# Kernel optimization log

Measured on AMD Instinct MI355X. Metric: run time of the kernel, lower is better.

The kernel has to match this reference:

```python
import jax, jax.numpy as jnp
import numpy as np
from jax import lax

# SRCNN: conv 9x9 (1->64) + ReLU, conv 5x5 (64->32) + ReLU, conv 5x5 (32->1), same padding.
# 13 units total: indices 0-3 (x2 stage), 4-7 (x4 stage), 8-11 (x8 stage), 12 (msf).

def _conv(x, w, b):
    y = lax.conv_general_dilated(x, w, window_strides=(1, 1), padding='SAME',
                                 dimension_numbers=('NCHW', 'OIHW', 'NCHW'))
    return y + b[None, :, None, None]


def _srcnn(x, w1, b1, w2, b2, w3, b3):
    h = jax.nn.relu(_conv(x, w1, b1))
    h = jax.nn.relu(_conv(h, w2, b2))
    return _conv(h, w3, b3)


def _interleave(p0, p1, p2, p3):
    # out[b,c,2h,2w]=p0, out[b,c,2h,2w+1]=p1, out[b,c,2h+1,2w]=p2, out[b,c,2h+1,2w+1]=p3
    B, C, H, W = p0.shape
    x = jnp.stack([jnp.stack([p0, p1], axis=-1),
                   jnp.stack([p2, p3], axis=-1)], axis=-2)  # (B,C,H,W,2,2) dims (b,c,h,w,r,s)
    x = x.transpose(0, 1, 2, 4, 3, 5)                        # (b,c,h,r,w,s)
    return x.reshape(B, C, 2 * H, 2 * W)


def _stage(x, off, W1, B1, W2, B2, W3, B3):
    outs = [_srcnn(x, W1[off + i], B1[off + i], W2[off + i], B2[off + i],
                   W3[off + i], B3[off + i]) for i in range(4)]
    return _interleave(*outs)


def _upscale(x, s):
    B, C, H, W = x.shape
    return jax.image.resize(x, (B, C, H * s, W * s), method='bilinear')


def setup_inputs() -> dict:
    key = jax.random.key(0)
    ks = jax.random.split(key, 7)
    image = jax.random.normal(ks[0], (4, 1, 64, 64), dtype=jnp.float32)
    n = 13
    W1 = jax.random.normal(ks[1], (n, 64, 1, 9, 9), dtype=jnp.float32) * 0.05
    B1 = jnp.zeros((n, 64), dtype=jnp.float32)
    W2 = jax.random.normal(ks[2], (n, 32, 64, 5, 5), dtype=jnp.float32) * 0.05
    B2 = jnp.zeros((n, 32), dtype=jnp.float32)
    W3 = jax.random.normal(ks[3], (n, 1, 32, 5, 5), dtype=jnp.float32) * 0.05
    B3 = jnp.zeros((n, 1), dtype=jnp.float32)
    return {'image': image, 'W1': W1, 'B1': B1, 'W2': W2, 'B2': B2, 'W3': W3, 'B3': B3}


def reference(image, W1, B1, W2, B2, W3, B3):
    out_x2 = _stage(image, 0, W1, B1, W2, B2, W3, B3)   # (B,1,128,128)
    out_x4 = _stage(out_x2, 4, W1, B1, W2, B2, W3, B3)  # (B,1,256,256)
    out_x8 = _stage(out_x4, 8, W1, B1, W2, B2, W3, B3)  # (B,1,512,512)
    msf_in = _upscale(out_x2, 4) + _upscale(out_x4, 2) + out_x8
    msf_out = _srcnn(msf_in, W1[12], B1[12], W2[12], B2[12], W3[12], B3[12])
    return (out_x2, out_x4, out_x8, msf_out)
```

## Files before the change

### kernel.cpp

```cpp
#include <hip/hip_runtime.h>


typedef unsigned short ushort_t;
typedef __attribute__((ext_vector_type(8))) short short8;
typedef __attribute__((ext_vector_type(4))) float f32x4;
typedef __attribute__((ext_vector_type(2))) unsigned int u32x2;

__device__ __forceinline__ float us2f(ushort_t u) { return __uint_as_float(((unsigned int)u) << 16); }
__device__ __forceinline__ ushort_t f2us(float f) {
    unsigned int x = __float_as_uint(f);
    return (ushort_t)((x + 0x7fffu + ((x >> 16) & 1u)) >> 16);
}
__device__ __forceinline__ unsigned int pk_bf16(float lo, float hi) {
    unsigned int r;
    asm("v_cvt_pk_bf16_f32 %0, %1, %2" : "=v"(r) : "v"(lo), "v"(hi));
    return r;
}

#define MFMA16(a, b, c) __builtin_amdgcn_mfma_f32_16x16x32_bf16((a), (b), (c), 0, 0, 0)

__global__ __launch_bounds__(256) void prep_weights(
    const float* __restrict__ W1, const float* __restrict__ W2, const float* __restrict__ W3,
    ushort_t* __restrict__ w1t, ushort_t* __restrict__ w2t, ushort_t* __restrict__ w3t)
{
    int i = blockIdx.x * 256 + threadIdx.x;
    if (i < 13 * 3 * 4 * 64 * 8) {
        int e = i & 7, ch = (i >> 3) & 63, cig = (i >> 9) & 3;
        int r = i >> 11;
        int kc = r % 3, u = r / 3;
        int tap = kc * 32 + e * 4 + cig;
        w1t[i] = (tap < 81) ? f2us(W1[(u * 64 + ch) * 81 + tap]) : (ushort_t)0;
    }
    if (i < 665600) {
        int e = i & 7, co = (i >> 3) & 31, cig = (i >> 8) & 3;
        int r = i >> 10;
        int s = r % 25, cc = r / 25;
        int dx = s / 5, dy = s - 5 * dx;
        int c = cc & 1, u = cc >> 1;
        int tap = dy * 5 + dx;
        int ci = c * 32 + cig * 8 + e;
        w2t[i] = f2us(W2[((u * 32 + co) * 64 + ci) * 25 + tap]);
    }
    if (i < 13 * 25 * 32) {
        int ci = i & 31, r = i >> 5;
        int tap = r % 25, u = r / 25;
        w3t[i] = f2us(W3[(u * 32 + ci) * 25 + tap]);
    }
}

__global__ __launch_bounds__(256, 2) void srcnn_mfma(
    const float* __restrict__ in, int H, int W,
    const ushort_t* __restrict__ w1t, const ushort_t* __restrict__ w2t,
    const ushort_t* __restrict__ w3t,
    const float* __restrict__ gB1, const float* __restrict__ gB2,
    const float* __restrict__ gB3,
    int unitBase, float* __restrict__ out, int s2)
{
    __shared__ __align__(16) char smem[52928];
    ushort_t* sH1  = (ushort_t*)smem;
    ushort_t* sInU = (ushort_t*)(smem + 51328);
    ushort_t* sW3  = (ushort_t*)(smem + 51328);
    ushort_t* sH2  = (ushort_t*)smem;

    const int t = threadIdx.x, lane = t & 63, wv = t >> 6;
    const int q = lane >> 4, l15 = lane & 15;
    const int z = blockIdx.z;
    const int k4 = (s2 == 2) ? (z >> 2) : 0;
    const int b  = (s2 == 2) ? (z & 3)  : z;
    const int unit = unitBase + k4;
    const int ppx = k4 & 1, ppy = k4 >> 1;
    const int ox0 = blockIdx.x * 12, oy0 = blockIdx.y * 12;
    const int outW = W * s2;
    const int outH = H * s2;
    const float* inb = in + (size_t)b * H * W;

    const char* w2u = (const char*)w2t + (size_t)unit * 102400;

    auto loadB5 = [&](short8* buf, int p, int n) {
        const char* g = w2u + (size_t)p * 10240 + q * 512 + (n * 16 + l15) * 16;
#pragma unroll
        for (int dy = 0; dy < 5; ++dy)
            buf[dy] = *(const short8*)(g + dy * 2048);
    };

    for (int idx = t; idx < 784; idx += 256) {
        int y = idx / 28, x = idx - 28 * y;
        int gy = oy0 - 8 + y, gx = ox0 - 8 + x;
        sInU[idx] = (gy >= 0 && gy < H && gx >= 0 && gx < W)
                    ? f2us(inb[(size_t)gy * W + gx]) : (ushort_t)0;
    }
    __syncthreads();

    const ushort_t* w1u = w1t + (size_t)unit * (3 * 4 * 64 * 8);

    f32x4 bias4[4];
#pragma unroll
    for (int n = 0; n < 4; ++n)
        bias4[n] = *(const f32x4*)&gB1[unit * 64 + n * 16 + q * 4];

#pragma unroll 1
    for (int ms = 0; ms < 2; ++ms) {
        const int mbase = ms * 16;
        const int nim = ms ? 3 : 4;
        f32x4 acc1h[4][4];
#pragma unroll
        for (int i = 0; i < 4; ++i)
#pragma unroll
            for (int n = 0; n < 4; ++n) acc1h[i][n] = (f32x4){0.f, 0.f, 0.f, 0.f};

#pragma unroll 1
        for (int kc = 0; kc < 3; ++kc) {
            short8 bh[4];
#pragma unroll
            for (int n = 0; n < 4; ++n)
                bh[n] = *(const short8*)&w1u[((kc * 4 + q) * 64 + n * 16 + l15) * 8];
            int toff8[8];
#pragma unroll
            for (int j = 0; j < 8; ++j) {
                int T = kc * 32 + j * 4 + q;
                int ty = (T * 57) >> 9;
                int o  = ty * 28 + (T - 9 * ty);
                toff8[j] = (T < 81) ? o : 0;
            }
#pragma unroll
            for (int im = 0; im < 4; ++im) {
                if (im < nim) {
                    int m = mbase + wv + im * 4;
                    if (m < 25) {
                        int px = m * 16 + l15;
                        int py1 = (px * 205) >> 12;
                        int base = py1 * 28 + (px - 20 * py1);
                        union { short8 v; ushort_t u[8]; } a;
#pragma unroll
                        for (int j = 0; j < 8; ++j)
                            a.u[j] = sInU[base + toff8[j]];
#pragma unroll
                        for (int n = 0; n < 4; ++n)
                            acc1h[im][n] = MFMA16(bh[n], a.v, acc1h[im][n]);
                    }
                }
            }
        }

#pragma unroll
        for (int im = 0; im < 4; ++im) {
            if (im < nim) {
                int m = mbase + wv + im * 4;
                if (m < 25) {
                    int px = m * 16 + l15;
                    int py1 = (px * 205) >> 12;
                    int px1 = px - 20 * py1;
                    int gy = oy0 - 4 + py1, gx = ox0 - 4 + px1;
                    bool ok = (gy >= 0 && gy < H && gx >= 0 && gx < W);
#pragma unroll
                    for (int n = 0; n < 4; ++n) {
                        float v0 = fmaxf(acc1h[im][n][0] + bias4[n][0], 0.f);
                        float v1 = fmaxf(acc1h[im][n][1] + bias4[n][1], 0.f);
                        float v2 = fmaxf(acc1h[im][n][2] + bias4[n][2], 0.f);
                        float v3 = fmaxf(acc1h[im][n][3] + bias4[n][3], 0.f);
                        unsigned int w0 = pk_bf16(v0, v1);
                        unsigned int w1 = pk_bf16(v2, v3);
                        if (!ok) { w0 = 0u; w1 = 0u; }
                        *(u32x2*)&sH1[(n * 2 + (q >> 1)) * 3208 + px * 8 + (q & 1) * 4]
                            = (u32x2){w0, w1};
                    }
                }
            }
        }
    }
    __syncthreads();

    {
        const ushort_t* w3u = w3t + unit * 800;
        for (int i = t; i < 800; i += 256) sW3[i] = w3u[i];
    }

    f32x4 acc2[4][2];
#pragma unroll
    for (int i = 0; i < 4; ++i) { acc2[i][0] = (f32x4){0.f,0.f,0.f,0.f}; acc2[i][1] = (f32x4){0.f,0.f,0.f,0.f}; }

#pragma unroll
    for (int c = 0; c < 2; ++c) {
        short8 Ba[10], Bb[10];
        loadB5(Ba,     c * 5, 0);
        loadB5(Ba + 5, c * 5, 1);
        const ushort_t* base = &sH1[(c * 4 + q) * 3208];
#pragma unroll
        for (int dx = 0; dx < 5; ++dx) {
            const short8* cur = (dx & 1) ? Bb : Ba;
            short8*       nxt = (dx & 1) ? Ba : Bb;
            if (dx < 4) {
                loadB5(nxt,     c * 5 + dx + 1, 0);
                loadB5(nxt + 5, c * 5 + dx + 1, 1);
            }
#pragma unroll
            for (int rel = 0; rel < 8; ++rel) {
                int row = wv * 4 + rel;
                short8 a = *(const short8*)&base[(row * 20 + l15 + dx) * 8];
                const int dylo = rel - 3 < 0 ? 0 : rel - 3;
                const int dyhi = rel < 4 ? rel : 4;
#pragma unroll
                for (int dy = 0; dy < 5; ++dy) {
                    if (dy >= dylo && dy <= dyhi) {
                        int im = rel - dy;
                        acc2[im][0] = MFMA16(cur[dy],     a, acc2[im][0]);
                        acc2[im][1] = MFMA16(cur[5 + dy], a, acc2[im][1]);
                    }
                }
            }
        }
    }
    __syncthreads();

    {
        f32x4 b2v[2];
#pragma unroll
        for (int n = 0; n < 2; ++n)
            b2v[n] = *(const f32x4*)&gB2[unit * 32 + n * 16 + q * 4];
        int gx = ox0 - 2 + l15;
        bool okx = (gx >= 0 && gx < W);
#pragma unroll
        for (int im = 0; im < 4; ++im) {
            int hy = wv * 4 + im;
            int gy = oy0 - 2 + hy;
            bool ok = okx && (gy >= 0 && gy < H);
#pragma unroll
            for (int n = 0; n < 2; ++n) {
                float v0 = fmaxf(acc2[im][n][0] + b2v[n][0], 0.f);
                float v1 = fmaxf(acc2[im][n][1] + b2v[n][1], 0.f);
                float v2 = fmaxf(acc2[im][n][2] + b2v[n][2], 0.f);
                float v3 = fmaxf(acc2[im][n][3] + b2v[n][3], 0.f);
                unsigned int w0 = pk_bf16(v0, v1);
                unsigned int w1 = pk_bf16(v2, v3);
                if (!ok) { w0 = 0u; w1 = 0u; }
                *(u32x2*)&sH2[(n * 2 + (q >> 1)) * 2064 + (hy * 16 + l15) * 8 + (q & 1) * 4]
                    = (u32x2){w0, w1};
            }
        }
    }
    __syncthreads();

    float b3 = gB3[unit];
    const int nm = (wv == 0) ? 3 : 2;
    int oyj[3], oxj[3];
#pragma unroll
    for (int jm = 0; jm < 3; ++jm) {
        int p = (wv + 4 * jm) * 16 + l15;
        oyj[jm] = (p * 683) >> 13;
        oxj[jm] = p - 12 * oyj[jm];
    }
    f32x4 acc3[3];
#pragma unroll
    for (int jm = 0; jm < 3; ++jm) acc3[jm] = (f32x4){0.f, 0.f, 0.f, 0.f};

#pragma unroll 1
    for (int tap = 0; tap < 25; ++tap) {
        int dy = (tap * 13) >> 6, dx = tap - 5 * dy;
        short8 w = *(const short8*)&sW3[tap * 32 + q * 8];
#pragma unroll
        for (int jm = 0; jm < 3; ++jm) {
            if (jm < nm) {
                int h2px = (oyj[jm] + dy) * 16 + oxj[jm] + dx;
                short8 a = *(const short8*)&sH2[q * 2064 + h2px * 8];
                acc3[jm] = MFMA16(a, w, acc3[jm]);
            }
        }
    }
    if (l15 == 0) {
#pragma unroll
        for (int jm = 0; jm < 3; ++jm) {
            if (jm < nm) {
                int mt = wv + 4 * jm;
#pragma unroll
                for (int r = 0; r < 4; ++r) {
                    int pp = mt * 16 + q * 4 + r;
                    int oy = (pp * 683) >> 13, ox = pp - 12 * oy;
                    int gy = oy0 + oy, gx = ox0 + ox;
                    if (gy < H && gx < W) {
                        size_t o = (size_t)b * outW * outH + (size_t)(gy * s2 + ppy) * outW + (gx * s2 + ppx);
                        out[o] = acc3[jm][r] + b3;
                    }
                }
            }
        }
    }
}

__device__ __forceinline__ void ax_w(int i, float inv_s, int n, int& i0, int& i1, float& w1) {
    float c  = (i + 0.5f) * inv_s - 0.5f;
    float fl = floorf(c);
    w1 = c - fl;
    int ii = (int)fl;
    i0 = ii < 0 ? 0 : ii;
    i1 = (ii + 1 >= n) ? (n - 1) : (ii + 1);
}

__global__ __launch_bounds__(256) void msf_in_kernel(
    const float* __restrict__ f2, const float* __restrict__ f4,
    const float* __restrict__ f8, float* __restrict__ dst)
{
    int idx = blockIdx.x * 256 + threadIdx.x;
    int x = idx & 511;
    int y = (idx >> 9) & 511;
    int b = idx >> 18;

    int y0, y1, x0, x1;
    float wy, wx;

    ax_w(y, 0.25f, 128, y0, y1, wy);
    ax_w(x, 0.25f, 128, x0, x1, wx);
    const float* p2 = f2 + (size_t)b * 16384;
    float v4 = (1.f - wy) * ((1.f - wx) * p2[y0 * 128 + x0] + wx * p2[y0 * 128 + x1])
             +        wy  * ((1.f - wx) * p2[y1 * 128 + x0] + wx * p2[y1 * 128 + x1]);

    ax_w(y, 0.5f, 256, y0, y1, wy);
    ax_w(x, 0.5f, 256, x0, x1, wx);
    const float* p4 = f4 + (size_t)b * 65536;
    float v2 = (1.f - wy) * ((1.f - wx) * p4[y0 * 256 + x0] + wx * p4[y0 * 256 + x1])
             +        wy  * ((1.f - wx) * p4[y1 * 256 + x0] + wx * p4[y1 * 256 + x1]);

    dst[idx] = v4 + v2 + f8[idx];
}

extern "C" void kernel_launch(void* const* d_in, const int* in_sizes, int n_in,
                              void* d_out, int out_size, void* d_ws, size_t ws_size,
                              hipStream_t stream)
{
    (void)in_sizes; (void)n_in; (void)out_size; (void)ws_size;

    const float* image = (const float*)d_in[0];
    const float* W1    = (const float*)d_in[1];
    const float* B1    = (const float*)d_in[2];
    const float* W2    = (const float*)d_in[3];
    const float* B2    = (const float*)d_in[4];
    const float* W3    = (const float*)d_in[5];
    const float* B3    = (const float*)d_in[6];

    float* out = (float*)d_out;
    float* o2 = out;
    float* o4 = out + 65536;
    float* o8 = out + 327680;
    float* om = out + 1376256;

    float*    fm  = (float*)d_ws;
    ushort_t* w1t = (ushort_t*)((char*)d_ws + 4194304);
    ushort_t* w2t = (ushort_t*)((char*)d_ws + 4354048);
    ushort_t* w3t = (ushort_t*)((char*)d_ws + 5685248);

    prep_weights<<<2600, 256, 0, stream>>>(W1, W2, W3, w1t, w2t, w3t);

    srcnn_mfma<<<dim3(6, 6, 16), 256, 0, stream>>>(
        image, 64, 64, w1t, w2t, w3t, B1, B2, B3, 0, o2, 2);
    srcnn_mfma<<<dim3(11, 11, 16), 256, 0, stream>>>(
        o2, 128, 128, w1t, w2t, w3t, B1, B2, B3, 4, o4, 2);
    srcnn_mfma<<<dim3(22, 22, 16), 256, 0, stream>>>(
        o4, 256, 256, w1t, w2t, w3t, B1, B2, B3, 8, o8, 2);
    msf_in_kernel<<<4096, 256, 0, stream>>>(o2, o4, o8, fm);
    srcnn_mfma<<<dim3(43, 43, 4), 256, 0, stream>>>(
        fm, 512, 512, w1t, w2t, w3t, B1, B2, B3, 12, om, 1);
}
```

Before: 636.8 us.

## Repack conv2 MFMA K dimension as channel-group by dx taps to cut iterations

Reorganizes the 5x5 64->32 convolution so each MFMA K-slice covers 8 input channels times 4 horizontal taps (dx=0..3), with a separate pass for the dx=4 column over the 64 channels. The weight prep kernel gets a matching new w2t layout. The loop goes from 10 K-blocks to 8+2, and the B operand is read from LDS with a per-quad dx offset. It relies on the LDS H1 layout putting 8 channels contiguously per pixel so shifted pixels can be gathered by lane quad. It adds index complexity and changes the weight streaming order.

```diff
diff --git a/kernel.cpp b/kernel.cpp
--- a/kernel.cpp
+++ b/kernel.cpp
@@ -31,15 +31,23 @@
         int tap = kc * 32 + e * 4 + cig;
         w1t[i] = (tap < 81) ? f2us(W1[(u * 64 + ch) * 81 + tap]) : (ushort_t)0;
     }
-    if (i < 665600) {
+    if (i < 532480) {
+        int e = i & 7, co = (i >> 3) & 31, qq = (i >> 8) & 3;
+        int b = i >> 10;
+        int dy = b % 5, tt = b / 5;
+        int c8 = tt % 8, u = tt / 8;
+        int ci = c8 * 8 + e;
+        int tap = dy * 5 + qq;
+        w2t[i] = f2us(W2[((u * 32 + co) * 64 + ci) * 25 + tap]);
+    }
+    if (i < 133120) {
         int e = i & 7, co = (i >> 3) & 31, cig = (i >> 8) & 3;
-        int r = i >> 10;
-        int s = r % 25, cc = r / 25;
-        int dx = s / 5, dy = s - 5 * dx;
-        int c = cc & 1, u = cc >> 1;
-        int tap = dy * 5 + dx;
+        int b = i >> 10;
+        int dy = b % 5, s = b / 5;
+        int c = s % 2, u = s / 2;
         int ci = c * 32 + cig * 8 + e;
-        w2t[i] = f2us(W2[((u * 32 + co) * 64 + ci) * 25 + tap]);
+        int tap = dy * 5 + 4;
+        w2t[532480 + i] = f2us(W2[((u * 32 + co) * 64 + ci) * 25 + tap]);
     }
     if (i < 13 * 25 * 32) {
         int ci = i & 31, r = i >> 5;
@@ -74,13 +82,16 @@
     const int outH = H * s2;
     const float* inb = in + (size_t)b * H * W;
 
-    const char* w2u = (const char*)w2t + (size_t)unit * 102400;
-
-    auto loadB5 = [&](short8* buf, int p, int n) {
-        const char* g = w2u + (size_t)p * 10240 + q * 512 + (n * 16 + l15) * 16;
-#pragma unroll
-        for (int dy = 0; dy < 5; ++dy)
-            buf[dy] = *(const short8*)(g + dy * 2048);
+    const char* w2m_u = (const char*)w2t + (size_t)unit * 81920;
+    const char* w2x_u = (const char*)w2t + 1064960 + (size_t)unit * 20480;
+
+    auto loadW = [&](short8* buf, const char* base, int blk) {
+        const char* g = base + (size_t)blk * 10240 + q * 512 + l15 * 16;
+#pragma unroll
+        for (int dy = 0; dy < 5; ++dy) {
+            buf[dy]     = *(const short8*)(g + dy * 2048);
+            buf[5 + dy] = *(const short8*)(g + dy * 2048 + 256);
+        }
     };
 
     for (int idx = t; idx < 784; idx += 256) {
@@ -179,32 +190,50 @@
 #pragma unroll
     for (int i = 0; i < 4; ++i) { acc2[i][0] = (f32x4){0.f,0.f,0.f,0.f}; acc2[i][1] = (f32x4){0.f,0.f,0.f,0.f}; }
 
-#pragma unroll
-    for (int c = 0; c < 2; ++c) {
-        short8 Ba[10], Bb[10];
-        loadB5(Ba,     c * 5, 0);
-        loadB5(Ba + 5, c * 5, 1);
-        const ushort_t* base = &sH1[(c * 4 + q) * 3208];
-#pragma unroll
-        for (int dx = 0; dx < 5; ++dx) {
-            const short8* cur = (dx & 1) ? Bb : Ba;
-            short8*       nxt = (dx & 1) ? Ba : Bb;
-            if (dx < 4) {
-                loadB5(nxt,     c * 5 + dx + 1, 0);
-                loadB5(nxt + 5, c * 5 + dx + 1, 1);
-            }
+    {
+        short8 Wa[10], Wb[10];
+        loadW(Wa, w2m_u, 0);
+#pragma unroll
+        for (int c8 = 0; c8 < 8; ++c8) {
+            const short8* cw = (c8 & 1) ? Wb : Wa;
+            short8*       nw = (c8 & 1) ? Wa : Wb;
+            if (c8 < 7) loadW(nw, w2m_u, c8 + 1);
+            else        loadW(nw, w2x_u, 0);
+            const ushort_t* bpl = &sH1[c8 * 3208];
 #pragma unroll
             for (int rel = 0; rel < 8; ++rel) {
                 int row = wv * 4 + rel;
-                short8 a = *(const short8*)&base[(row * 20 + l15 + dx) * 8];
+                short8 bf = *(const short8*)&bpl[(row * 20 + l15 + q) * 8];
                 const int dylo = rel - 3 < 0 ? 0 : rel - 3;
                 const int dyhi = rel < 4 ? rel : 4;
 #pragma unroll
                 for (int dy = 0; dy < 5; ++dy) {
                     if (dy >= dylo && dy <= dyhi) {
                         int im = rel - dy;
-                        acc2[im][0] = MFMA16(cur[dy],     a, acc2[im][0]);
-                        acc2[im][1] = MFMA16(cur[5 + dy], a, acc2[im][1]);
+                        acc2[im][0] = MFMA16(cw[dy],     bf, acc2[im][0]);
+                        acc2[im][1] = MFMA16(cw[5 + dy], bf, acc2[im][1]);
+                    }
+                }
+            }
+        }
+#pragma unroll
+        for (int c = 0; c < 2; ++c) {
+            const short8* cw = (c & 1) ? Wb : Wa;
+            short8*       nw = (c & 1) ? Wa : Wb;
+            if (c == 0) loadW(nw, w2x_u, 1);
+            const ushort_t* base = &sH1[(c * 4 + q) * 3208];
+#pragma unroll
+            for (int rel = 0; rel < 8; ++rel) {
+                int row = wv * 4 + rel;
+                short8 bf = *(const short8*)&base[(row * 20 + l15 + 4) * 8];
+                const int dylo = rel - 3 < 0 ? 0 : rel - 3;
+                const int dyhi = rel < 4 ? rel : 4;
+#pragma unroll
+                for (int dy = 0; dy < 5; ++dy) {
+                    if (dy >= dylo && dy <= dyhi) {
+                        int im = rel - dy;
+                        acc2[im][0] = MFMA16(cw[dy],     bf, acc2[im][0]);
+                        acc2[im][1] = MFMA16(cw[5 + dy], bf, acc2[im][1]);
                     }
                 }
             }
```

After: 626.1 us. No clear change (-1.7%).
